# Kernel tuning notes

Measured on AMD Instinct MI355X. Metric: run time of the kernel, lower is better.

## Reference

```python
import jax, jax.numpy as jnp
import numpy as np

HIDDEN = 512
B, H, W = 8, 48, 48
SCALE = 1.0 / np.sqrt(HIDDEN).astype(np.float32)


def conv1x1(x, w, b):
    # x: [B, C, H, W], w: [O, C], b: [O]  (1x1 Conv2d == channel matmul)
    return jnp.einsum('bchw,oc->bohw', x, w) + b[None, :, None, None]


def setup_inputs() -> dict:
    key = jax.random.key(0)
    ks = jax.random.split(key, 10)
    s = 1.0 / np.sqrt(HIDDEN)
    return {
        'locx': jax.random.normal(ks[0], (B, HIDDEN, H, W), dtype=jnp.float32),
        'glox': jax.random.normal(ks[1], (B, HIDDEN, H, W), dtype=jnp.float32),
        'Wq': jax.random.normal(ks[2], (HIDDEN, HIDDEN), dtype=jnp.float32) * s,
        'bq': jax.random.normal(ks[3], (HIDDEN,), dtype=jnp.float32) * 0.01,
        'Wk': jax.random.normal(ks[4], (HIDDEN, HIDDEN), dtype=jnp.float32) * s,
        'bk': jax.random.normal(ks[5], (HIDDEN,), dtype=jnp.float32) * 0.01,
        'Wv': jax.random.normal(ks[6], (HIDDEN, HIDDEN), dtype=jnp.float32) * s,
        'bv': jax.random.normal(ks[7], (HIDDEN,), dtype=jnp.float32) * 0.01,
        'Wo': jax.random.normal(ks[8], (HIDDEN, HIDDEN), dtype=jnp.float32) * s,
        'bo': jax.random.normal(ks[9], (HIDDEN,), dtype=jnp.float32) * 0.01,
    }


def reference(locx, glox, Wq, bq, Wk, bk, Wv, bv, Wo, bo):
    b, c, h, w = locx.shape
    # 1x1 conv projections
    q = conv1x1(locx, Wq, bq).reshape(b, c, h * w)   # [B, C, N]
    k = conv1x1(glox, Wk, bk).reshape(b, c, -1)      # [B, C, M]
    v = conv1x1(glox, Wv, bv).reshape(b, c, -1)      # [B, C, M]
    # scores = Q^T K / sqrt(hidden)  -> [B, N, M]
    scores = jnp.einsum('bcn,bcm->bnm', q, k) * SCALE
    probs = jax.nn.softmax(scores, axis=-1)           # dropout rate 0.0 -> identity
    # context = probs @ V^T -> [B, N, C] -> [B, C, H, H]
    ctx = jnp.einsum('bnm,bcm->bcn', probs, v).reshape(b, c, h, h)
    out = conv1x1(ctx, Wo, bo)                        # proj dropout 0.0 -> identity
    return out
```

## Files before the change

### kernel.cpp

```cpp
#include <hip/hip_runtime.h>
#include <hip/hip_bf16.h>

typedef __attribute__((ext_vector_type(4))) float f32x4;
typedef __attribute__((ext_vector_type(8))) short bf16x8;
typedef __attribute__((ext_vector_type(4))) short s16x4;

#define C_DIM 512
#define N_PIX 2304
#define N_BATCH 8
#define ATT_SCALE 0.04419417382415922f
#define NJB 18

typedef __attribute__((address_space(3))) unsigned int lds_u32;
typedef const __attribute__((address_space(1))) unsigned int glob_u32;

__device__ __forceinline__ void gl2lds16(const __hip_bfloat16* g, __hip_bfloat16* l)
{
    __builtin_amdgcn_global_load_lds((glob_u32*)g, (lds_u32*)l, 16, 0, 0);
}

template<int OUT_BF16, int BIAS_MODE, int EPI, int NJ, int NS, int IFAST, int NI>
__global__ __launch_bounds__(256)
void gemm_bt(const __hip_bfloat16* __restrict__ A, const __hip_bfloat16* __restrict__ B,
             void* __restrict__ Dp, const float* __restrict__ bias,
             float* __restrict__ rsum,
             float scale, int K, int lda, int ldb, int ldd,
             long sA, long sB, long sD)
{
    __shared__ __hip_bfloat16 As[128 * 64];
    __shared__ __hip_bfloat16 Bs[128 * 64];

    const int lin = blockIdx.x;
    const int s   = lin % NS;
    const int t   = lin / NS;
    const int bz  = s;
    int ib, jb;
    if (IFAST) { ib = t % NI; jb = t / NI; }
    else       { jb = t % NJ; ib = t / NJ; }
    const int i0 = ib * 128;
    const int j0 = jb * 128;

    const int tid  = threadIdx.x;
    const int lane = tid & 63;
    const int wave = tid >> 6;

    const __hip_bfloat16* Ab = A + (size_t)bz * (size_t)sA;
    const __hip_bfloat16* Bb = B + (size_t)bz * (size_t)sB;
    __hip_bfloat16* D16 = (__hip_bfloat16*)Dp + (size_t)bz * (size_t)sD;
    float*          D32 = (float*)Dp          + (size_t)bz * (size_t)sD;

    const int lrow = lane >> 3;
    const int lcs  = (lane & 7) ^ lrow;
    const __hip_bfloat16* ga = Ab + (size_t)(i0 + wave * 32 + lrow) * lda + lcs * 8;
    const __hip_bfloat16* gb = Bb + (size_t)(j0 + wave * 32 + lrow) * ldb + lcs * 8;
    __hip_bfloat16* la = As + wave * 32 * 64;
    __hip_bfloat16* lb = Bs + wave * 32 * 64;

    const int fr = lane & 15;
    const int fq = lane >> 4;
    const int sw = fr & 7;
    const int wi = (wave >> 1) * 64;
    const int wj = (wave & 1) * 64;

    f32x4 acc[4][4];
#pragma unroll
    for (int a = 0; a < 4; ++a)
#pragma unroll
        for (int b = 0; b < 4; ++b)
            acc[a][b] = (f32x4){0.f, 0.f, 0.f, 0.f};

    for (int k0 = 0; k0 < K; k0 += 64) {
#pragma unroll
        for (int ss = 0; ss < 4; ++ss) {
            gl2lds16(ga + (size_t)ss * 8 * lda + k0, la + ss * 8 * 64);
            gl2lds16(gb + (size_t)ss * 8 * ldb + k0, lb + ss * 8 * 64);
        }
        __syncthreads();

#pragma unroll
        for (int kk = 0; kk < 2; ++kk) {
            bf16x8 af[4], bfr[4];
            const int ca = ((kk * 4 + fq) ^ sw) << 3;
#pragma unroll
            for (int tt = 0; tt < 4; ++tt) {
                af[tt]  = *(const bf16x8*)(&As[(wi + tt * 16 + fr) * 64 + ca]);
                bfr[tt] = *(const bf16x8*)(&Bs[(wj + tt * 16 + fr) * 64 + ca]);
            }
#pragma unroll
            for (int a = 0; a < 4; ++a)
#pragma unroll
                for (int b = 0; b < 4; ++b)
                    acc[a][b] = __builtin_amdgcn_mfma_f32_16x16x32_bf16(
                        af[a], bfr[b], acc[a][b], 0, 0, 0);
        }
        __syncthreads();
    }

    const int orow = fq * 4;

    float rjv[4];
    if (EPI == 3) {
        const float* ri = rsum + (size_t)bz * N_PIX;
#pragma unroll
        for (int b = 0; b < 4; ++b)
            rjv[b] = ri[j0 + wj + b * 16 + fr];
    }

    float rpart[4][4];
    if (EPI == 1) {
#pragma unroll
        for (int a = 0; a < 4; ++a)
#pragma unroll
            for (int r = 0; r < 4; ++r)
                rpart[a][r] = 0.f;
    }

#pragma unroll
    for (int a = 0; a < 4; ++a) {
        int ibx = i0 + wi + a * 16 + orow;
#pragma unroll
        for (int b = 0; b < 4; ++b) {
            int j = j0 + wj + b * 16 + fr;
            float bj = (BIAS_MODE == 2) ? bias[j] : 0.f;
#pragma unroll
            for (int r = 0; r < 4; ++r) {
                int i = ibx + r;
                float v = acc[a][b][r] * scale;
                if (EPI == 3) v *= rjv[b];
                if (BIAS_MODE == 1) v += bias[i];
                if (BIAS_MODE == 2) v += bj;
                if (EPI == 1) { v = __expf(v); rpart[a][r] += v; }
                if (OUT_BF16)
                    D16[(size_t)i * ldd + j] = __float2bfloat16(v);
                else
                    D32[(size_t)i * ldd + j] = v;
            }
        }
    }

    if (EPI == 1) {
#pragma unroll
        for (int m = 1; m < 16; m <<= 1)
#pragma unroll
            for (int a = 0; a < 4; ++a)
#pragma unroll
                for (int r = 0; r < 4; ++r)
                    rpart[a][r] += __shfl_xor(rpart[a][r], m);
        float* rsl = (float*)As;
        if (fr == 0) {
#pragma unroll
            for (int a = 0; a < 4; ++a)
#pragma unroll
                for (int r = 0; r < 4; ++r)
                    rsl[wave * 64 + a * 16 + orow + r] = rpart[a][r];
        }
        __syncthreads();
        if (tid < 128) {
            int half = tid >> 6, rr = tid & 63;
            float sm = rsl[(half * 2) * 64 + rr] + rsl[(half * 2 + 1) * 64 + rr];
            rsum[((size_t)jb * N_BATCH + bz) * N_PIX + i0 + tid] = sm;
        }
    }
}

__global__ __launch_bounds__(256)
void proj_qkv(const __hip_bfloat16* __restrict__ Xl,
              const __hip_bfloat16* __restrict__ Xg,
              const __hip_bfloat16* __restrict__ wgt,
              const float* __restrict__ bq, const float* __restrict__ bk,
              const float* __restrict__ bv,
              __hip_bfloat16* __restrict__ QKV)
{
    __shared__ __hip_bfloat16 As[128 * 64];
    __shared__ __hip_bfloat16 Bs[128 * 64];

    const int lin = blockIdx.x;
    const int s   = lin % 24;
    const int bz  = s & 7;
    const int mat = s >> 3;
    const int t   = lin / 24;
    const int j0  = (t & 3) * 128;
    const int i0  = (t >> 2) * 128;

    const __hip_bfloat16* Ab = ((mat == 0) ? Xl : Xg) + (size_t)bz * N_PIX * C_DIM;
    const __hip_bfloat16* Bb = wgt + (size_t)mat * C_DIM * C_DIM;
    const float* bias = (mat == 0) ? bq : (mat == 1) ? bk : bv;
    __hip_bfloat16* D = QKV + ((size_t)mat * N_BATCH + bz) * N_PIX * C_DIM;

    const int tid  = threadIdx.x;
    const int lane = tid & 63;
    const int wave = tid >> 6;

    const int lrow = lane >> 3;
    const int lcs  = (lane & 7) ^ lrow;
    const __hip_bfloat16* ga = Ab + (size_t)(i0 + wave * 32 + lrow) * C_DIM + lcs * 8;
    const __hip_bfloat16* gb = Bb + (size_t)(j0 + wave * 32 + lrow) * C_DIM + lcs * 8;
    __hip_bfloat16* la = As + wave * 32 * 64;
    __hip_bfloat16* lb = Bs + wave * 32 * 64;

    const int fr = lane & 15;
    const int fq = lane >> 4;
    const int sw = fr & 7;
    const int wi = (wave >> 1) * 64;
    const int wj = (wave & 1) * 64;

    f32x4 acc[4][4];
#pragma unroll
    for (int a = 0; a < 4; ++a)
#pragma unroll
        for (int b = 0; b < 4; ++b)
            acc[a][b] = (f32x4){0.f, 0.f, 0.f, 0.f};

    for (int k0 = 0; k0 < C_DIM; k0 += 64) {
#pragma unroll
        for (int ss = 0; ss < 4; ++ss) {
            gl2lds16(ga + (size_t)ss * 8 * C_DIM + k0, la + ss * 8 * 64);
            gl2lds16(gb + (size_t)ss * 8 * C_DIM + k0, lb + ss * 8 * 64);
        }
        __syncthreads();

#pragma unroll
        for (int kk = 0; kk < 2; ++kk) {
            bf16x8 af[4], bfr[4];
            const int ca = ((kk * 4 + fq) ^ sw) << 3;
#pragma unroll
            for (int tt = 0; tt < 4; ++tt) {
                af[tt]  = *(const bf16x8*)(&As[(wi + tt * 16 + fr) * 64 + ca]);
                bfr[tt] = *(const bf16x8*)(&Bs[(wj + tt * 16 + fr) * 64 + ca]);
            }
#pragma unroll
            for (int a = 0; a < 4; ++a)
#pragma unroll
                for (int b = 0; b < 4; ++b)
                    acc[a][b] = __builtin_amdgcn_mfma_f32_16x16x32_bf16(
                        af[a], bfr[b], acc[a][b], 0, 0, 0);
        }
        __syncthreads();
    }

    const int orow = fq * 4;
#pragma unroll
    for (int a = 0; a < 4; ++a) {
        int ibx = i0 + wi + a * 16 + orow;
#pragma unroll
        for (int b = 0; b < 4; ++b) {
            int j = j0 + wj + b * 16 + fr;
            float bj = bias[j];
#pragma unroll
            for (int r = 0; r < 4; ++r)
                D[(size_t)(ibx + r) * C_DIM + j] = __float2bfloat16(acc[a][b][r] + bj);
        }
    }
}

__global__ __launch_bounds__(256)
void reduce_rinv(const float* __restrict__ rp, float* __restrict__ rinv)
{
    int idx = blockIdx.x * 256 + threadIdx.x;
    float s = 0.f;
#pragma unroll
    for (int jb = 0; jb < NJB; ++jb)
        s += rp[(size_t)jb * N_BATCH * N_PIX + idx];
    rinv[idx] = 1.f / s;
}

__global__ __launch_bounds__(256)
void transpose_cast(const float* __restrict__ locx, const float* __restrict__ glox,
                    __hip_bfloat16* __restrict__ Xl, __hip_bfloat16* __restrict__ Xg)
{
    __shared__ float t[64 * 65];
    const int n0 = blockIdx.x * 64;
    const int c0 = blockIdx.y * 64;
    const int z  = blockIdx.z;
    const size_t b = z & 7;
    const float* Xb = ((z < 8) ? locx : glox) + b * (size_t)C_DIM * N_PIX;
    __hip_bfloat16* Xt = (z < 8) ? Xl : Xg;
    const int tid = threadIdx.x;

    const int n_l = tid & 63;
    const int c_b = tid >> 6;
#pragma unroll
    for (int s = 0; s < 16; ++s) {
        int c_l = c_b + s * 4;
        t[c_l * 65 + n_l] = Xb[(size_t)(c0 + c_l) * N_PIX + n0 + n_l];
    }
    __syncthreads();

    const int cc = (tid & 7) * 8;
    const int nb = tid >> 3;
#pragma unroll
    for (int it = 0; it < 2; ++it) {
        int n2 = nb + it * 32;
        union { __hip_bfloat16 h[8]; int4 v; } u;
#pragma unroll
        for (int w = 0; w < 8; ++w)
            u.h[w] = __float2bfloat16(t[(cc + w) * 65 + n2]);
        *(int4*)(&Xt[(b * N_PIX + n0 + n2) * C_DIM + c0 + cc]) = u.v;
    }
}

__global__ __launch_bounds__(256)
void cast_w4(const float* __restrict__ s0, const float* __restrict__ s1,
             const float* __restrict__ s2, const float* __restrict__ s3,
             __hip_bfloat16* __restrict__ dst)
{
    const float* srcs[4] = {s0, s1, s2, s3};
    const int w = blockIdx.y;
    const int i = (blockIdx.x * 256 + threadIdx.x) * 4;
    float4 f = *(const float4*)(srcs[w] + i);
    union { __hip_bfloat16 h[4]; s16x4 q; } t;
    t.h[0] = __float2bfloat16(f.x);
    t.h[1] = __float2bfloat16(f.y);
    t.h[2] = __float2bfloat16(f.z);
    t.h[3] = __float2bfloat16(f.w);
    *(s16x4*)(dst + (size_t)w * C_DIM * C_DIM + i) = t.q;
}

extern "C" void kernel_launch(void* const* d_in, const int* in_sizes, int n_in,
                              void* d_out, int out_size, void* d_ws, size_t ws_size,
                              hipStream_t stream)
{
    const float* locx = (const float*)d_in[0];
    const float* glox = (const float*)d_in[1];
    const float* Wq = (const float*)d_in[2];
    const float* bq = (const float*)d_in[3];
    const float* Wk = (const float*)d_in[4];
    const float* bk = (const float*)d_in[5];
    const float* Wv = (const float*)d_in[6];
    const float* bv = (const float*)d_in[7];
    const float* Wo = (const float*)d_in[8];
    const float* bo = (const float*)d_in[9];
    float* out = (float*)d_out;

    const int C = C_DIM, N = N_PIX;
    const size_t WB   = (size_t)C * C * 2;
    const size_t szX  = (size_t)N_BATCH * N * C * 2;
    const size_t szP1 = (size_t)N * N * 2;
    const size_t szRP = (size_t)NJB * N_BATCH * N * 4;
    const size_t szRI = (size_t)N_BATCH * N * 4;

    const size_t fixed = 4 * WB + 6 * szX + szRP + szRI;
    bool full = (ws_size >= fixed + 8 * szP1 + 4096);

    char* ws = (char*)d_ws;
    size_t off = 0;
    auto alloc = [&](size_t bytes) {
        char* p = ws + off;
        off += (bytes + 255) & ~(size_t)255;
        return p;
    };
    __hip_bfloat16* wgt = (__hip_bfloat16*)alloc(4 * WB);
    __hip_bfloat16* Xl  = (__hip_bfloat16*)alloc(szX);
    __hip_bfloat16* Xg  = (__hip_bfloat16*)alloc(szX);
    __hip_bfloat16* QKV = (__hip_bfloat16*)alloc(3 * szX);
    __hip_bfloat16* Vp  = (__hip_bfloat16*)alloc(szX);
    float*          rp   = (float*)alloc(szRP);
    float*          rinv = (float*)alloc(szRI);
    __hip_bfloat16* Pu  = (__hip_bfloat16*)alloc(full ? 8 * szP1 : szP1);

    __hip_bfloat16* Qt = QKV;
    __hip_bfloat16* Kt = QKV + (size_t)N_BATCH * N * C;
    __hip_bfloat16* Vt = QKV + 2 * (size_t)N_BATCH * N * C;
    __hip_bfloat16* wo_b = wgt + 3 * (size_t)C * C;

    const dim3 blk(256);
    const long sPr = (long)N * C;
    const long sCN = (long)C * N;

    cast_w4<<<dim3(C * C / 1024, 4), blk, 0, stream>>>(Wq, Wk, Wv, Wo, wgt);
    transpose_cast<<<dim3(N / 64, C / 64, 16), blk, 0, stream>>>(locx, glox, Xl, Xg);

    proj_qkv<<<dim3(24 * 72), blk, 0, stream>>>(Xl, Xg, wgt, bq, bk, bv, QKV);

    if (full) {
        gemm_bt<1, 0, 1, 18, 8, 0, 0><<<dim3(18 * 18 * 8), blk, 0, stream>>>(
            Qt, Kt, Pu, nullptr, rp,
            ATT_SCALE, C, C, C, N, sPr, sPr, (long)N * N);
        gemm_bt<1, 0, 0, 18, 8, 1, 4><<<dim3(4 * 18 * 8), blk, 0, stream>>>(
            wo_b, Vt, Vp, nullptr, nullptr,
            1.f, C, C, C, N, 0, sPr, sCN);
        reduce_rinv<<<dim3(8 * N / 256), blk, 0, stream>>>(rp, rinv);
        gemm_bt<0, 1, 3, 18, 8, 1, 4><<<dim3(4 * 18 * 8), blk, 0, stream>>>(
            Vp, Pu, out, bo, rinv,
            1.f, N, N, N, N, sCN, (long)N * N, sCN);
    } else {
        gemm_bt<1, 0, 0, 18, 8, 1, 4><<<dim3(4 * 18 * 8), blk, 0, stream>>>(
            wo_b, Vt, Vp, nullptr, nullptr,
            1.f, C, C, C, N, 0, sPr, sCN);
        for (int r = 0; r < N_BATCH; ++r) {
            gemm_bt<1, 0, 1, 18, 1, 0, 0><<<dim3(18 * 18), blk, 0, stream>>>(
                Qt + (size_t)r * sPr, Kt + (size_t)r * sPr, Pu, nullptr,
                rp + (size_t)r * N,
                ATT_SCALE, C, C, C, N, 0, 0, 0);
            reduce_rinv<<<dim3(N / 256), blk, 0, stream>>>(
                rp + (size_t)r * N, rinv + (size_t)r * N);
            gemm_bt<0, 1, 3, 18, 1, 1, 4><<<dim3(4 * 18), blk, 0, stream>>>(
                Vp + (size_t)r * sCN, Pu, out + (size_t)r * sCN, bo,
                rinv + (size_t)r * N,
                1.f, N, N, N, N, 0, 0, 0);
        }
    }
}
```

Baseline: 339.8 us.

## Fuse prep kernels, merge score and V-projection GEMMs, fold row-sum reduction into PV

```diff
diff --git a/kernel.cpp b/kernel.cpp
--- a/kernel.cpp
+++ b/kernel.cpp
@@ -19,24 +19,40 @@
     __builtin_amdgcn_global_load_lds((glob_u32*)g, (lds_u32*)l, 16, 0, 0);
 }
 
-template<int OUT_BF16, int BIAS_MODE, int EPI, int NJ, int NS, int IFAST, int NI>
+template<int NS>
 __global__ __launch_bounds__(256)
-void gemm_bt(const __hip_bfloat16* __restrict__ A, const __hip_bfloat16* __restrict__ B,
-             void* __restrict__ Dp, const float* __restrict__ bias,
-             float* __restrict__ rsum,
-             float scale, int K, int lda, int ldb, int ldd,
-             long sA, long sB, long sD)
+void s_vp(const __hip_bfloat16* __restrict__ Qt, const __hip_bfloat16* __restrict__ Kt,
+          __hip_bfloat16* __restrict__ Pu, float* __restrict__ rp,
+          const __hip_bfloat16* __restrict__ wo, const __hip_bfloat16* __restrict__ Vt,
+          __hip_bfloat16* __restrict__ Vp, int bz_off, long sPu)
 {
     __shared__ __hip_bfloat16 As[128 * 64];
     __shared__ __hip_bfloat16 Bs[128 * 64];
 
     const int lin = blockIdx.x;
-    const int s   = lin % NS;
+    const int bz  = lin % NS + bz_off;
     const int t   = lin / NS;
-    const int bz  = s;
+    const bool is_s = (t < 324);
+
     int ib, jb;
-    if (IFAST) { ib = t % NI; jb = t / NI; }
-    else       { jb = t % NJ; ib = t / NJ; }
+    const __hip_bfloat16 *A, *B;
+    __hip_bfloat16* D;
+    float scale;
+    const long sQ = (long)N_PIX * C_DIM;
+    if (is_s) {
+        ib = t / 18; jb = t % 18;
+        A = Qt + (size_t)bz * sQ;
+        B = Kt + (size_t)bz * sQ;
+        D = Pu + (size_t)bz * (size_t)sPu;
+        scale = ATT_SCALE;
+    } else {
+        int u = t - 324;
+        ib = u / 18; jb = u % 18;
+        A = wo;
+        B = Vt + (size_t)bz * sQ;
+        D = Vp + (size_t)bz * sQ;
+        scale = 1.f;
+    }
     const int i0 = ib * 128;
     const int j0 = jb * 128;
 
@@ -44,15 +60,10 @@
     const int lane = tid & 63;
     const int wave = tid >> 6;
 
-    const __hip_bfloat16* Ab = A + (size_t)bz * (size_t)sA;
-    const __hip_bfloat16* Bb = B + (size_t)bz * (size_t)sB;
-    __hip_bfloat16* D16 = (__hip_bfloat16*)Dp + (size_t)bz * (size_t)sD;
-    float*          D32 = (float*)Dp          + (size_t)bz * (size_t)sD;
-
     const int lrow = lane >> 3;
     const int lcs  = (lane & 7) ^ lrow;
-    const __hip_bfloat16* ga = Ab + (size_t)(i0 + wave * 32 + lrow) * lda + lcs * 8;
-    const __hip_bfloat16* gb = Bb + (size_t)(j0 + wave * 32 + lrow) * ldb + lcs * 8;
+    const __hip_bfloat16* ga = A + (size_t)(i0 + wave * 32 + lrow) * C_DIM + lcs * 8;
+    const __hip_bfloat16* gb = B + (size_t)(j0 + wave * 32 + lrow) * C_DIM + lcs * 8;
     __hip_bfloat16* la = As + wave * 32 * 64;
     __hip_bfloat16* lb = Bs + wave * 32 * 64;
 
@@ -69,11 +80,11 @@
         for (int b = 0; b < 4; ++b)
             acc[a][b] = (f32x4){0.f, 0.f, 0.f, 0.f};
 
-    for (int k0 = 0; k0 < K; k0 += 64) {
+    for (int k0 = 0; k0 < C_DIM; k0 += 64) {
 #pragma unroll
         for (int ss = 0; ss < 4; ++ss) {
-            gl2lds16(ga + (size_t)ss * 8 * lda + k0, la + ss * 8 * 64);
-            gl2lds16(gb + (size_t)ss * 8 * ldb + k0, lb + ss * 8 * 64);
+            gl2lds16(ga + (size_t)ss * 8 * C_DIM + k0, la + ss * 8 * 64);
+            gl2lds16(gb + (size_t)ss * 8 * C_DIM + k0, lb + ss * 8 * 64);
         }
         __syncthreads();
 
@@ -98,47 +109,27 @@
 
     const int orow = fq * 4;
 
-    float rjv[4];
-    if (EPI == 3) {
-        const float* ri = rsum + (size_t)bz * N_PIX;
-#pragma unroll
-        for (int b = 0; b < 4; ++b)
-            rjv[b] = ri[j0 + wj + b * 16 + fr];
-    }
-
-    float rpart[4][4];
-    if (EPI == 1) {
+    if (is_s) {
+        float rpart[4][4];
 #pragma unroll
         for (int a = 0; a < 4; ++a)
 #pragma unroll
             for (int r = 0; r < 4; ++r)
                 rpart[a][r] = 0.f;
-    }
-
-#pragma unroll
-    for (int a = 0; a < 4; ++a) {
-        int ibx = i0 + wi + a * 16 + orow;
-#pragma unroll
-        for (int b = 0; b < 4; ++b) {
-            int j = j0 + wj + b * 16 + fr;
-            float bj = (BIAS_MODE == 2) ? bias[j] : 0.f;
-#pragma unroll
-            for (int r = 0; r < 4; ++r) {
-                int i = ibx + r;
-                float v = acc[a][b][r] * scale;
-                if (EPI == 3) v *= rjv[b];
-                if (BIAS_MODE == 1) v += bias[i];
-                if (BIAS_MODE == 2) v += bj;
-                if (EPI == 1) { v = __expf(v); rpart[a][r] += v; }
-                if (OUT_BF16)
-                    D16[(size_t)i * ldd + j] = __float2bfloat16(v);
-                else
-                    D32[(size_t)i * ldd + j] = v;
+#pragma unroll
+        for (int a = 0; a < 4; ++a) {
+            int ibx = i0 + wi + a * 16 + orow;
+#pragma unroll
+            for (int b = 0; b < 4; ++b) {
+                int j = j0 + wj + b * 16 + fr;
+#pragma unroll
+                for (int r = 0; r < 4; ++r) {
+                    float v = __expf(acc[a][b][r] * scale);
+                    rpart[a][r] += v;
+                    D[(size_t)(ibx + r) * N_PIX + j] = __float2bfloat16(v);
+                }
             }
         }
-    }
-
-    if (EPI == 1) {
 #pragma unroll
         for (int m = 1; m < 16; m <<= 1)
 #pragma unroll
@@ -158,7 +149,121 @@
         if (tid < 128) {
             int half = tid >> 6, rr = tid & 63;
             float sm = rsl[(half * 2) * 64 + rr] + rsl[(half * 2 + 1) * 64 + rr];
-            rsum[((size_t)jb * N_BATCH + bz) * N_PIX + i0 + tid] = sm;
+            rp[((size_t)jb * N_BATCH + bz) * N_PIX + i0 + tid] = sm;
+        }
+    } else {
+#pragma unroll
+        for (int a = 0; a < 4; ++a) {
+            int ibx = i0 + wi + a * 16 + orow;
+#pragma unroll
+            for (int b = 0; b < 4; ++b) {
+                int j = j0 + wj + b * 16 + fr;
+#pragma unroll
+                for (int r = 0; r < 4; ++r)
+                    D[(size_t)(ibx + r) * N_PIX + j] = __float2bfloat16(acc[a][b][r]);
+            }
+        }
+    }
+}
+
+template<int NS>
+__global__ __launch_bounds__(256)
+void pv_out(const __hip_bfloat16* __restrict__ Vp, const __hip_bfloat16* __restrict__ Pu,
+            float* __restrict__ out, const float* __restrict__ bo,
+            const float* __restrict__ rp, int bz_off, long sPu)
+{
+    __shared__ __hip_bfloat16 As[64 * 64];
+    __shared__ __hip_bfloat16 Bs[128 * 64];
+
+    const int lin = blockIdx.x;
+    const int bz  = lin % NS + bz_off;
+    const int t   = lin / NS;
+    const int ib  = t % 8;
+    const int jb  = t / 8;
+    const int i0  = ib * 64;
+    const int j0  = jb * 128;
+
+    const long sCN = (long)C_DIM * N_PIX;
+    const __hip_bfloat16* A = Vp + (size_t)bz * sCN;
+    const __hip_bfloat16* B = Pu + (size_t)bz * (size_t)sPu;
+    float* D = out + (size_t)bz * sCN;
+
+    const int tid  = threadIdx.x;
+    const int lane = tid & 63;
+    const int wave = tid >> 6;
+
+    const int lrow = lane >> 3;
+    const int lcs  = (lane & 7) ^ lrow;
+    const __hip_bfloat16* ga = A + (size_t)(i0 + wave * 16 + lrow) * N_PIX + lcs * 8;
+    const __hip_bfloat16* gb = B + (size_t)(j0 + wave * 32 + lrow) * N_PIX + lcs * 8;
+    __hip_bfloat16* la = As + wave * 16 * 64;
+    __hip_bfloat16* lb = Bs + wave * 32 * 64;
+
+    const int fr = lane & 15;
+    const int fq = lane >> 4;
+    const int sw = fr & 7;
+    const int wi = (wave >> 1) * 32;
+    const int wj = (wave & 1) * 64;
+
+    f32x4 acc[2][4];
+#pragma unroll
+    for (int a = 0; a < 2; ++a)
+#pragma unroll
+        for (int b = 0; b < 4; ++b)
+            acc[a][b] = (f32x4){0.f, 0.f, 0.f, 0.f};
+
+    for (int k0 = 0; k0 < N_PIX; k0 += 64) {
+#pragma unroll
+        for (int ss = 0; ss < 2; ++ss)
+            gl2lds16(ga + (size_t)ss * 8 * N_PIX + k0, la + ss * 8 * 64);
+#pragma unroll
+        for (int ss = 0; ss < 4; ++ss)
+            gl2lds16(gb + (size_t)ss * 8 * N_PIX + k0, lb + ss * 8 * 64);
+        __syncthreads();
+
+#pragma unroll
+        for (int kk = 0; kk < 2; ++kk) {
+            bf16x8 af[2], bfr[4];
+            const int ca = ((kk * 4 + fq) ^ sw) << 3;
+#pragma unroll
+            for (int tt = 0; tt < 2; ++tt)
+                af[tt]  = *(const bf16x8*)(&As[(wi + tt * 16 + fr) * 64 + ca]);
+#pragma unroll
+            for (int tt = 0; tt < 4; ++tt)
+                bfr[tt] = *(const bf16x8*)(&Bs[(wj + tt * 16 + fr) * 64 + ca]);
+#pragma unroll
+            for (int a = 0; a < 2; ++a)
+#pragma unroll
+                for (int b = 0; b < 4; ++b)
+                    acc[a][b] = __builtin_amdgcn_mfma_f32_16x16x32_bf16(
+                        af[a], bfr[b], acc[a][b], 0, 0, 0);
+        }
+        __syncthreads();
+    }
+
+    const int orow = fq * 4;
+    float rjv[4];
+#pragma unroll
+    for (int b = 0; b < 4; ++b) {
+        int j = j0 + wj + b * 16 + fr;
+        float s = 0.f;
+#pragma unroll
+        for (int jj = 0; jj < NJB; ++jj)
+            s += rp[((size_t)jj * N_BATCH + bz) * N_PIX + j];
+        rjv[b] = 1.f / s;
+    }
+
+#pragma unroll
+    for (int a = 0; a < 2; ++a) {
+        int ibx = i0 + wi + a * 16 + orow;
+#pragma unroll
+        for (int r = 0; r < 4; ++r) {
+            float bi = bo[ibx + r];
+#pragma unroll
+            for (int b = 0; b < 4; ++b) {
+                int j = j0 + wj + b * 16 + fr;
+                D[(size_t)(ibx + r) * N_PIX + j] = acc[a][b][r] * rjv[b] + bi;
+            }
         }
     }
 }
@@ -254,66 +359,58 @@
 }
 
 __global__ __launch_bounds__(256)
-void reduce_rinv(const float* __restrict__ rp, float* __restrict__ rinv)
-{
-    int idx = blockIdx.x * 256 + threadIdx.x;
-    float s = 0.f;
-#pragma unroll
-    for (int jb = 0; jb < NJB; ++jb)
-        s += rp[(size_t)jb * N_BATCH * N_PIX + idx];
-    rinv[idx] = 1.f / s;
-}
-
-__global__ __launch_bounds__(256)
-void transpose_cast(const float* __restrict__ locx, const float* __restrict__ glox,
-                    __hip_bfloat16* __restrict__ Xl, __hip_bfloat16* __restrict__ Xg)
-{
-    __shared__ float t[64 * 65];
-    const int n0 = blockIdx.x * 64;
-    const int c0 = blockIdx.y * 64;
-    const int z  = blockIdx.z;
-    const size_t b = z & 7;
-    const float* Xb = ((z < 8) ? locx : glox) + b * (size_t)C_DIM * N_PIX;
-    __hip_bfloat16* Xt = (z < 8) ? Xl : Xg;
+void prep(const float* __restrict__ locx, const float* __restrict__ glox,
+          __hip_bfloat16* __restrict__ Xl, __hip_bfloat16* __restrict__ Xg,
+          const float* __restrict__ w0, const float* __restrict__ w1,
+          const float* __restrict__ w2, const float* __restrict__ w3,
+          __hip_bfloat16* __restrict__ wgt)
+{
+    const int lin = blockIdx.x;
     const int tid = threadIdx.x;
 
-    const int n_l = tid & 63;
-    const int c_b = tid >> 6;
-#pragma unroll
-    for (int s = 0; s < 16; ++s) {
-        int c_l = c_b + s * 4;
-        t[c_l * 65 + n_l] = Xb[(size_t)(c0 + c_l) * N_PIX + n0 + n_l];
-    }
-    __syncthreads();
-
-    const int cc = (tid & 7) * 8;
-    const int nb = tid >> 3;
-#pragma unroll
-    for (int it = 0; it < 2; ++it) {
-        int n2 = nb + it * 32;
-        union { __hip_bfloat16 h[8]; int4 v; } u;
-#pragma unroll
-        for (int w = 0; w < 8; ++w)
-            u.h[w] = __float2bfloat16(t[(cc + w) * 65 + n2]);
-        *(int4*)(&Xt[(b * N_PIX + n0 + n2) * C_DIM + c0 + cc]) = u.v;
-    }
-}
-
-__global__ __launch_bounds__(256)
-void cast_w4(const float* __restrict__ s0, const float* __restrict__ s1,
-             const float* __restrict__ s2, const float* __restrict__ s3,
-             __hip_bfloat16* __restrict__ dst)
-{
-    const float* srcs[4] = {s0, s1, s2, s3};
-    const int w = blockIdx.y;
-    const int i = (blockIdx.x * 256 + threadIdx.x) * 4;
-    float4 f = *(const float4*)(srcs[w] + i);
-    union { __hip_bfloat16 h[4]; s16x4 q; } t;
-    t.h[0] = __float2bfloat16(f.x);
-    t.h[1] = __float2bfloat16(f.y);
-    t.h[2] = __float2bfloat16(f.z);
-    t.h[3] = __float2bfloat16(f.w);
-    *(s16x4*)(dst + (size_t)w * C_DIM * C_DIM + i) = t.q;
+    if (lin < 4608) {
+        __shared__ float t[64 * 65];
+        const int z  = lin & 15;
+        const int t2 = lin >> 4;
+        const int c0 = (t2 & 7) * 64;
+        const int n0 = (t2 >> 3) * 64;
+        const size_t b = z & 7;
+        const float* Xb = ((z < 8) ? locx : glox) + b * (size_t)C_DIM * N_PIX;
+        __hip_bfloat16* Xt = (z < 8) ? Xl : Xg;
+
+        const int n_l = tid & 63;
+        const int c_b = tid >> 6;
+#pragma unroll
+        for (int s = 0; s < 16; ++s) {
+            int c_l = c_b + s * 4;
+            t[c_l * 65 + n_l] = Xb[(size_t)(c0 + c_l) * N_PIX + n0 + n_l];
+        }
+        __syncthreads();
+
+        const int cc = (tid & 7) * 8;
+        const int nb = tid >> 3;
+#pragma unroll
+        for (int it = 0; it < 2; ++it) {
+            int n2 = nb + it * 32;
+            union { __hip_bfloat16 h[8]; int4 v; } u;
+#pragma unroll
+            for (int w = 0; w < 8; ++w)
+                u.h[w] = __float2bfloat16(t[(cc + w) * 65 + n2]);
+            *(int4*)(&Xt[(b * N_PIX + n0 + n2) * C_DIM + c0 + cc]) = u.v;
+        }
+    } else {
+        const int idx = lin - 4608;
+        const int w   = idx >> 8;
+        const float* srcs[4] = {w0, w1, w2, w3};
+        const int i = ((idx & 255) * 256 + tid) * 4;
+        float4 f = *(const float4*)(srcs[w] + i);
+        union { __hip_bfloat16 h[4]; s16x4 q; } u;
+        u.h[0] = __float2bfloat16(f.x);
+        u.h[1] = __float2bfloat16(f.y);
+        u.h[2] = __float2bfloat16(f.z);
+        u.h[3] = __float2bfloat16(f.w);
+        *(s16x4*)(wgt + (size_t)w * C_DIM * C_DIM + i) = u.q;
+    }
 }
 
 extern "C" void kernel_launch(void* const* d_in, const int* in_sizes, int n_in,
@@ -337,9 +434,8 @@
     const size_t szX  = (size_t)N_BATCH * N * C * 2;
     const size_t szP1 = (size_t)N * N * 2;
     const size_t szRP = (size_t)NJB * N_BATCH * N * 4;
-    const size_t szRI = (size_t)N_BATCH * N * 4;
-
-    const size_t fixed = 4 * WB + 6 * szX + szRP + szRI;
+
+    const size_t fixed = 4 * WB + 6 * szX + szRP;
     bool full = (ws_size >= fixed + 8 * szP1 + 4096);
 
     char* ws = (char*)d_ws;
@@ -354,8 +450,7 @@
     __hip_bfloat16* Xg  = (__hip_bfloat16*)alloc(szX);
     __hip_bfloat16* QKV = (__hip_bfloat16*)alloc(3 * szX);
     __hip_bfloat16* Vp  = (__hip_bfloat16*)alloc(szX);
-    float*          rp   = (float*)alloc(szRP);
-    float*          rinv = (float*)alloc(szRI);
+    float*          rp  = (float*)alloc(szRP);
     __hip_bfloat16* Pu  = (__hip_bfloat16*)alloc(full ? 8 * szP1 : szP1);
 
     __hip_bfloat16* Qt = QKV;
@@ -364,40 +459,21 @@
     __hip_bfloat16* wo_b = wgt + 3 * (size_t)C * C;
 
     const dim3 blk(256);
-    const long sPr = (long)N * C;
-    const long sCN = (long)C * N;
-
-    cast_w4<<<dim3(C * C / 1024, 4), blk, 0, stream>>>(Wq, Wk, Wv, Wo, wgt);
-    transpose_cast<<<dim3(N / 64, C / 64, 16), blk, 0, stream>>>(locx, glox, Xl, Xg);
-
+
+    prep<<<dim3(5632), blk, 0, stream>>>(locx, glox, Xl, Xg, Wq, Wk, Wv, Wo, wgt);
     proj_qkv<<<dim3(24 * 72), blk, 0, stream>>>(Xl, Xg, wgt, bq, bk, bv, QKV);
 
     if (full) {
-        gemm_bt<1, 0, 1, 18, 8, 0, 0><<<dim3(18 * 18 * 8), blk, 0, stream>>>(
-            Qt, Kt, Pu, nullptr, rp,
-            ATT_SCALE, C, C, C, N, sPr, sPr, (long)N * N);
-        gemm_bt<1, 0, 0, 18, 8, 1, 4><<<dim3(4 * 18 * 8), blk, 0, stream>>>(
-            wo_b, Vt, Vp, nullptr, nullptr,
-            1.f, C, C, C, N, 0, sPr, sCN);
-        reduce_rinv<<<dim3(8 * N / 256), blk, 0, stream>>>(rp, rinv);
-        gemm_bt<0, 1, 3, 18, 8, 1, 4><<<dim3(4 * 18 * 8), blk, 0, stream>>>(
-            Vp, Pu, out, bo, rinv,
-            1.f, N, N, N, N, sCN, (long)N * N, sCN);
+        s_vp<8><<<dim3(8 * 396), blk, 0, stream>>>(
+            Qt, Kt, Pu, rp, wo_b, Vt, Vp, 0, (long)N * N);
+        pv_out<8><<<dim3(8 * 144), blk, 0, stream>>>(
+            Vp, Pu, out, bo, rp, 0, (long)N * N);
     } else {
-        gemm_bt<1, 0, 0, 18, 8, 1, 4><<<dim3(4 * 18 * 8), blk, 0, stream>>>(
-            wo_b, Vt, Vp, nullptr, nullptr,
-            1.f, C, C, C, N, 0, sPr, sCN);
         for (int r = 0; r < N_BATCH; ++r) {
-            gemm_bt<1, 0, 1, 18, 1, 0, 0><<<dim3(18 * 18), blk, 0, stream>>>(
-                Qt + (size_t)r * sPr, Kt + (size_t)r * sPr, Pu, nullptr,
-                rp + (size_t)r * N,
-                ATT_SCALE, C, C, C, N, 0, 0, 0);
-            reduce_rinv<<<dim3(N / 256), blk, 0, stream>>>(
-                rp + (size_t)r * N, rinv + (size_t)r * N);
-            gemm_bt<0, 1, 3, 18, 1, 1, 4><<<dim3(4 * 18), blk, 0, stream>>>(
-                Vp + (size_t)r * sCN, Pu, out + (size_t)r * sCN, bo,
-                rinv + (size_t)r * N,
-                1.f, N, N, N, N, 0, 0, 0);
-        }
-    }
-}
+            s_vp<1><<<dim3(396), blk, 0, stream>>>(
+                Qt, Kt, Pu, rp, wo_b, Vt, Vp, r, 0);
+            pv_out<1><<<dim3(144), blk, 0, stream>>>(
+                Vp, Pu, out, bo, rp, r, 0);
+        }
+    }
+}
```

Result: faster. 312.9 us (-7.9%).
